# Optimization experiments

Hardware: AMD Instinct MI355X
Metric: run time of the kernel (lower is better)

The kernel has to match this reference:

```python
import jax, jax.numpy as jnp
import numpy as np

IM_H, IM_W = 128, 128
HT_H, HT_W = 184, 180
N_VOTES = 1_500_000
B, C = 4, 32


def setup_inputs() -> dict:
    key = jax.random.key(0)
    k1, k2, k3, k4 = jax.random.split(key, 4)
    input_im = jax.random.normal(k1, (B, C, IM_H, IM_W), dtype=jnp.float32)
    im_idx = jax.random.randint(k2, (N_VOTES,), 0, IM_H * IM_W, dtype=jnp.int32)
    ht_idx = jax.random.randint(k3, (N_VOTES,), 0, HT_H * HT_W, dtype=jnp.int32)
    weight = jax.random.uniform(k4, (N_VOTES,), dtype=jnp.float32)
    return {"input_im": input_im, "im_idx": im_idx, "ht_idx": ht_idx, "weight": weight}


def reference(input_im, im_idx, ht_idx, weight):
    # input_im: [B, C, H, W] -> flatten pixels
    b, c, h, w = input_im.shape
    x = input_im.reshape(b, c, h * w)
    # gather voting pixel values and apply vote weights: [B, C, N]
    votes = x[:, :, im_idx] * weight  # broadcast weight over B, C
    # scatter-add into Hough bins (segment over leading axis)
    data = votes.transpose(2, 0, 1).reshape(votes.shape[2], b * c)  # [N, B*C]
    ht = jax.ops.segment_sum(data, ht_idx, num_segments=HT_H * HT_W)  # [HT, B*C]
    out = ht.T.reshape(b, c, HT_H, HT_W)
    return out
```

## Files before the change

### kernel.cpp

```cpp
#include <hip/hip_runtime.h>


#define HW   16384
#define BC   128
#define NHT  33120
#define RB   60
#define NB   552
#define CAPB 3712
#define CAPR 3528
#define VPB  4096
#define OFL_CAP 8192

typedef int iv4 __attribute__((ext_vector_type(4)));

__device__ __forceinline__ unsigned short f2bf(float f) {
  unsigned int u = __float_as_uint(f);
  u = (u + 0x7fff + ((u >> 16) & 1)) >> 16;
  return (unsigned short)u;
}

__global__ void k_zero(int* __restrict__ gcur, int* __restrict__ ofl_cnt) {
  int i = blockIdx.x * blockDim.x + threadIdx.x;
  if (i < NB) gcur[i] = 0;
  if (i == NB) *ofl_cnt = 0;
}

__global__ void k_transpose_in(const float* __restrict__ in,
                               unsigned short* __restrict__ xTh) {
  __shared__ float tile[32][33];
  int hw0 = blockIdx.x * 32, bc0 = blockIdx.y * 32;
  int tx = threadIdx.x, ty = threadIdx.y;
#pragma unroll
  for (int k = 0; k < 32; k += 8)
    tile[ty + k][tx] = in[(size_t)(bc0 + ty + k) * HW + hw0 + tx];
  __syncthreads();
#pragma unroll
  for (int k = 0; k < 32; k += 8)
    xTh[(size_t)(hw0 + ty + k) * BC + bc0 + tx] = f2bf(tile[tx][ty + k]);
}

__global__ __launch_bounds__(1024) void k_bucket(
    const int* __restrict__ im, const int* __restrict__ ht,
    const float* __restrict__ wt, int n,
    int* __restrict__ gcur, int2* __restrict__ bkt,
    int* __restrict__ ofl_cnt, int2* __restrict__ ofl) {
  __shared__ int cnt[NB];
  __shared__ int base[NB];
  int tid = threadIdx.x;
  int i0 = blockIdx.x * VPB;
  for (int b = tid; b < NB; b += 1024) cnt[b] = 0;
  __syncthreads();
  int hv[4];
#pragma unroll
  for (int k = 0; k < 4; ++k) {
    int i = i0 + k * 1024 + tid;
    hv[k] = (i < n) ? ht[i] : -1;
    if (i < n) atomicAdd(&cnt[hv[k] / RB], 1);
  }
  __syncthreads();
  for (int b = tid; b < NB; b += 1024) {
    int c = cnt[b];
    base[b] = c ? atomicAdd(&gcur[b], c) : 0;
    cnt[b] = 0;
  }
  __syncthreads();
#pragma unroll
  for (int k = 0; k < 4; ++k) {
    int i = i0 + k * 1024 + tid;
    if (i < n) {
      int h = hv[k];
      int b = h / RB;
      int hl = h - b * RB;
      int pos = base[b] + atomicAdd(&cnt[b], 1);
      if (pos < CAPR) {
        bkt[(size_t)b * CAPB + pos] =
            make_int2((im[i] & 0x3FFF) | (hl << 14), __float_as_int(wt[i]));
      } else {
        int o = atomicAdd(ofl_cnt, 1);
        if (o < OFL_CAP)
          ofl[o] = make_int2((im[i] & 0x3FFF) | (h << 14), __float_as_int(wt[i]));
      }
    }
  }
}

__global__ __launch_bounds__(512) void k_resort(
    const int2* __restrict__ bkt, const int* __restrict__ gcur,
    int2* __restrict__ fsorted, int* __restrict__ foffs, int* __restrict__ fcnt) {
  __shared__ int2 buf[CAPB];
  __shared__ int hist[RB];
  __shared__ int off[RB];
  int r = blockIdx.x, tid = threadIdx.x;
  int n = gcur[r];
  if (n > CAPR) n = CAPR;
  const int2* s = bkt + (size_t)r * CAPB;
  for (int i = tid; i < n; i += 512) buf[i] = s[i];
  if (tid < RB) hist[tid] = 0;
  __syncthreads();
  for (int i = tid; i < n; i += 512)
    atomicAdd(&hist[buf[i].x >> 14], 1);
  __syncthreads();
  if (tid == 0) {
    int run = 0;
    for (int b = 0; b < RB; ++b) { off[b] = run; run += (hist[b] + 3) & ~3; }
  }
  __syncthreads();
  if (tid < RB) {
    int padded = (hist[tid] + 3) & ~3;
    foffs[r * RB + tid] = r * CAPB + off[tid];
    fcnt[r * RB + tid] = padded;
    for (int d = hist[tid]; d < padded; ++d)
      fsorted[(size_t)r * CAPB + off[tid] + d] = make_int2(0, 0);
    hist[tid] = 0;
  }
  __syncthreads();
  for (int i = tid; i < n; i += 512) {
    int2 v = buf[i];
    int hl = v.x >> 14;
    int pos = off[hl] + atomicAdd(&hist[hl], 1);
    fsorted[(size_t)r * CAPB + pos] = make_int2(v.x & 0x3FFF, v.y);
  }
}

__device__ __forceinline__ void pick4(iv4 a, iv4 b, int q, int& im, float& w) {
  int imx = (q & 2) ? b.x : a.x;
  int imz = (q & 2) ? b.z : a.z;
  im = (q & 1) ? imz : imx;
  int wx = (q & 2) ? b.y : a.y;
  int wz = (q & 2) ? b.w : a.w;
  w = __int_as_float((q & 1) ? wz : wx);
}

__global__ __launch_bounds__(256) void k_accum5(
    const int2* __restrict__ fsorted, const int* __restrict__ foffs,
    const int* __restrict__ fcnt, const unsigned short* __restrict__ xTh,
    float* __restrict__ outT) {
  int gid = blockIdx.x * blockDim.x + threadIdx.x;
  int bin = __builtin_amdgcn_readfirstlane(gid >> 6);
  if (bin >= NHT) return;
  int lane = threadIdx.x & 63;
  int q = lane >> 4;
  int cg = lane & 15;
  int start = foffs[bin], n = fcnt[bin];
  const int* s = (const int*)(fsorted + start);
  const unsigned short* xb = xTh + (cg << 3);
  float acc[8] = {0, 0, 0, 0, 0, 0, 0, 0};

#define GATHER_FMA(IM, W)                                                     \
  {                                                                           \
    iv4 xd = *(const iv4*)(xb + ((size_t)(IM) << 7));                         \
    _Pragma("unroll") for (int c = 0; c < 4; ++c) {                           \
      float lo = __uint_as_float(((unsigned int)xd[c]) << 16);                \
      float hi = __uint_as_float(((unsigned int)xd[c]) & 0xffff0000u);        \
      acc[2 * c]     = fmaf((W), lo, acc[2 * c]);                             \
      acc[2 * c + 1] = fmaf((W), hi, acc[2 * c + 1]);                         \
    }                                                                         \
  }

  int i = 0;
  for (; i + 8 <= n; i += 8) {
    iv4 r0 = __builtin_nontemporal_load((const iv4*)(s + 2 * i));
    iv4 r1 = __builtin_nontemporal_load((const iv4*)(s + 2 * i + 4));
    iv4 r2 = __builtin_nontemporal_load((const iv4*)(s + 2 * i + 8));
    iv4 r3 = __builtin_nontemporal_load((const iv4*)(s + 2 * i + 12));
    int im0; float w0; pick4(r0, r1, q, im0, w0);
    int im1; float w1; pick4(r2, r3, q, im1, w1);
    GATHER_FMA(im0, w0);
    GATHER_FMA(im1, w1);
  }
  for (; i < n; i += 4) {
    iv4 r0 = __builtin_nontemporal_load((const iv4*)(s + 2 * i));
    iv4 r1 = __builtin_nontemporal_load((const iv4*)(s + 2 * i + 4));
    int im0; float w0; pick4(r0, r1, q, im0, w0);
    GATHER_FMA(im0, w0);
  }
#undef GATHER_FMA

  float r[8];
#pragma unroll
  for (int k = 0; k < 8; ++k) {
    float t = acc[k] + __shfl_xor(acc[k], 16);
    r[k] = t + __shfl_xor(t, 32);
  }
  if (lane < 16) {
    float4 lo = {r[0], r[1], r[2], r[3]};
    float4 hi = {r[4], r[5], r[6], r[7]};
    float4* dst = (float4*)(outT + ((size_t)bin << 7) + (cg << 3));
    __builtin_nontemporal_store(lo.x, &((float*)dst)[0]);
    __builtin_nontemporal_store(lo.y, &((float*)dst)[1]);
    __builtin_nontemporal_store(lo.z, &((float*)dst)[2]);
    __builtin_nontemporal_store(lo.w, &((float*)dst)[3]);
    __builtin_nontemporal_store(hi.x, &((float*)dst)[4]);
    __builtin_nontemporal_store(hi.y, &((float*)dst)[5]);
    __builtin_nontemporal_store(hi.z, &((float*)dst)[6]);
    __builtin_nontemporal_store(hi.w, &((float*)dst)[7]);
  }
}

__global__ void k_transpose_out(const float* __restrict__ outT, float* __restrict__ out) {
  __shared__ float tile[32][33];
  int ht0 = blockIdx.x * 32, bc0 = blockIdx.y * 32;
  int tx = threadIdx.x, ty = threadIdx.y;
#pragma unroll
  for (int k = 0; k < 32; k += 8)
    tile[ty + k][tx] = outT[(size_t)(ht0 + ty + k) * BC + bc0 + tx];
  __syncthreads();
#pragma unroll
  for (int k = 0; k < 32; k += 8)
    out[(size_t)(bc0 + ty + k) * NHT + ht0 + tx] = tile[tx][ty + k];
}

__global__ void k_overflow(const int* __restrict__ ofl_cnt, const int2* __restrict__ ofl,
                           const unsigned short* __restrict__ xTh,
                           float* __restrict__ out) {
  int cnt = *ofl_cnt;
  if (cnt > OFL_CAP) cnt = OFL_CAP;
  int c = threadIdx.x;
  for (int v = blockIdx.x; v < cnt; v += gridDim.x) {
    int2 rec = ofl[v];
    int imv = rec.x & 0x3FFF, h = rec.x >> 14;
    float wv = __int_as_float(rec.y);
    float xv = __uint_as_float(((unsigned int)xTh[((size_t)imv << 7) + c]) << 16);
    atomicAdd(&out[(size_t)c * NHT + h], wv * xv);
  }
}

extern "C" void kernel_launch(void* const* d_in, const int* in_sizes, int n_in,
                              void* d_out, int out_size, void* d_ws, size_t ws_size,
                              hipStream_t stream) {
  const float* input_im = (const float*)d_in[0];
  const int*   im_idx   = (const int*)d_in[1];
  const int*   ht_idx   = (const int*)d_in[2];
  const float* weight   = (const float*)d_in[3];
  float*       out      = (float*)d_out;
  const int N = in_sizes[1];

  char* w = (char*)d_ws;
  unsigned short* xTh = (unsigned short*)(w + 0);
  int2*  bkt     = (int2*) (w + 4194304);
  int2*  fsorted = (int2*) (w + 20586496);
  float* outT    = (float*)(w + 36978688);
  int*   foffs   = (int*)  (w + 53936128);
  int*   fcnt    = (int*)  (w + 54068608);
  int*   gcur    = (int*)  (w + 54201088);
  int*   ofl_cnt = (int*)  (w + 54203392);
  int2*  ofl     = (int2*) (w + 54203520);

  k_zero<<<(NB + 256) / 256, 256, 0, stream>>>(gcur, ofl_cnt);
  k_transpose_in<<<dim3(HW / 32, BC / 32), dim3(32, 8), 0, stream>>>(input_im, xTh);
  k_bucket<<<(N + VPB - 1) / VPB, 1024, 0, stream>>>(im_idx, ht_idx, weight, N,
                                                     gcur, bkt, ofl_cnt, ofl);
  k_resort<<<NB, 512, 0, stream>>>(bkt, gcur, fsorted, foffs, fcnt);
  k_accum5<<<NHT * 64 / 256, 256, 0, stream>>>(fsorted, foffs, fcnt, xTh, outT);
  k_transpose_out<<<dim3(NHT / 32, BC / 32), dim3(32, 8), 0, stream>>>(outT, out);
  k_overflow<<<16, BC, 0, stream>>>(ofl_cnt, ofl, xTh, out);
}
```

Measured before the change: 152.9 us.

## Fuse accumulation with output transpose and overflow handling; merge zero and transpose-in

Merges the zeroing kernel into the input transpose kernel as an extra block. The accumulation kernel now handles 32 bins per block, collects the results in shared memory and writes the final [BC, NHT] layout directly. This removes the outT intermediate, the transpose-out kernel and the overflow kernel, cutting two launches and a round trip of roughly 17MB through memory. In exchange, every block scans the whole overflow list serially whenever it is non-empty, and there are fewer and larger blocks, each running 4 bins per wave in sequence, which reduces load balance.

After: 161.7 us. 1.06x slower.

```diff
diff --git a/kernel.cpp b/kernel.cpp
--- a/kernel.cpp
+++ b/kernel.cpp
@@ -19,16 +19,16 @@
   return (unsigned short)u;
 }
 
-__global__ void k_zero(int* __restrict__ gcur, int* __restrict__ ofl_cnt) {
-  int i = blockIdx.x * blockDim.x + threadIdx.x;
-  if (i < NB) gcur[i] = 0;
-  if (i == NB) *ofl_cnt = 0;
-}
-
-__global__ void k_transpose_in(const float* __restrict__ in,
-                               unsigned short* __restrict__ xTh) {
+__global__ void k_init(const float* __restrict__ in, unsigned short* __restrict__ xTh,
+                       int* __restrict__ gcur, int* __restrict__ ofl_cnt) {
+  if (blockIdx.x == 2048) {
+    int tid = threadIdx.y * 32 + threadIdx.x;
+    for (int i = tid; i < NB; i += 256) gcur[i] = 0;
+    if (tid == 0) *ofl_cnt = 0;
+    return;
+  }
   __shared__ float tile[32][33];
-  int hw0 = blockIdx.x * 32, bc0 = blockIdx.y * 32;
+  int hw0 = (blockIdx.x & 511) * 32, bc0 = (blockIdx.x >> 9) * 32;
   int tx = threadIdx.x, ty = threadIdx.y;
 #pragma unroll
   for (int k = 0; k < 32; k += 8)
@@ -131,20 +131,26 @@
   w = __int_as_float((q & 1) ? wz : wx);
 }
 
-__global__ __launch_bounds__(256) void k_accum5(
+__global__ __launch_bounds__(512) void k_accum6(
     const int2* __restrict__ fsorted, const int* __restrict__ foffs,
     const int* __restrict__ fcnt, const unsigned short* __restrict__ xTh,
-    float* __restrict__ outT) {
-  int gid = blockIdx.x * blockDim.x + threadIdx.x;
-  int bin = __builtin_amdgcn_readfirstlane(gid >> 6);
-  if (bin >= NHT) return;
-  int lane = threadIdx.x & 63;
+    float* __restrict__ out, const int* __restrict__ ofl_cnt,
+    const int2* __restrict__ ofl) {
+  __shared__ float lacc[32 * 129];
+  int tid = threadIdx.x;
+  int ht0 = blockIdx.x * 32;
+  int w = __builtin_amdgcn_readfirstlane(tid >> 6);
+  int lane = tid & 63;
   int q = lane >> 4;
   int cg = lane & 15;
-  int start = foffs[bin], n = fcnt[bin];
-  const int* s = (const int*)(fsorted + start);
   const unsigned short* xb = xTh + (cg << 3);
-  float acc[8] = {0, 0, 0, 0, 0, 0, 0, 0};
+
+#pragma unroll
+  for (int bi = 0; bi < 4; ++bi) {
+    int bin = ht0 + w * 4 + bi;
+    int start = foffs[bin], n = fcnt[bin];
+    const int* s = (const int*)(fsorted + start);
+    float acc[8] = {0, 0, 0, 0, 0, 0, 0, 0};
 
 #define GATHER_FMA(IM, W)                                                     \
   {                                                                           \
@@ -157,71 +163,61 @@
     }                                                                         \
   }
 
-  int i = 0;
-  for (; i + 8 <= n; i += 8) {
-    iv4 r0 = __builtin_nontemporal_load((const iv4*)(s + 2 * i));
-    iv4 r1 = __builtin_nontemporal_load((const iv4*)(s + 2 * i + 4));
-    iv4 r2 = __builtin_nontemporal_load((const iv4*)(s + 2 * i + 8));
-    iv4 r3 = __builtin_nontemporal_load((const iv4*)(s + 2 * i + 12));
-    int im0; float w0; pick4(r0, r1, q, im0, w0);
-    int im1; float w1; pick4(r2, r3, q, im1, w1);
-    GATHER_FMA(im0, w0);
-    GATHER_FMA(im1, w1);
-  }
-  for (; i < n; i += 4) {
-    iv4 r0 = __builtin_nontemporal_load((const iv4*)(s + 2 * i));
-    iv4 r1 = __builtin_nontemporal_load((const iv4*)(s + 2 * i + 4));
-    int im0; float w0; pick4(r0, r1, q, im0, w0);
-    GATHER_FMA(im0, w0);
-  }
+    int i = 0;
+    for (; i + 8 <= n; i += 8) {
+      iv4 r0 = __builtin_nontemporal_load((const iv4*)(s + 2 * i));
+      iv4 r1 = __builtin_nontemporal_load((const iv4*)(s + 2 * i + 4));
+      iv4 r2 = __builtin_nontemporal_load((const iv4*)(s + 2 * i + 8));
+      iv4 r3 = __builtin_nontemporal_load((const iv4*)(s + 2 * i + 12));
+      int im0; float w0; pick4(r0, r1, q, im0, w0);
+      int im1; float w1; pick4(r2, r3, q, im1, w1);
+      GATHER_FMA(im0, w0);
+      GATHER_FMA(im1, w1);
+    }
+    for (; i < n; i += 4) {
+      iv4 r0 = __builtin_nontemporal_load((const iv4*)(s + 2 * i));
+      iv4 r1 = __builtin_nontemporal_load((const iv4*)(s + 2 * i + 4));
+      int im0; float w0; pick4(r0, r1, q, im0, w0);
+      GATHER_FMA(im0, w0);
+    }
 #undef GATHER_FMA
 
-  float r[8];
+#pragma unroll
+    for (int k = 0; k < 8; ++k) {
+      float t = acc[k] + __shfl_xor(acc[k], 16);
+      acc[k] = t + __shfl_xor(t, 32);
+    }
+    if (lane < 16) {
+      int row = (w * 4 + bi) * 129 + (cg << 3);
+#pragma unroll
+      for (int k = 0; k < 8; ++k) lacc[row + k] = acc[k];
+    }
+  }
+  __syncthreads();
+
+  int cnt = *ofl_cnt;
+  if (cnt > 0) {
+    if (cnt > OFL_CAP) cnt = OFL_CAP;
+    if (tid < 128) {
+      for (int v = 0; v < cnt; ++v) {
+        int2 rec = ofl[v];
+        int h = rec.x >> 14;
+        if (h >= ht0 && h < ht0 + 32) {
+          int imv = rec.x & 0x3FFF;
+          float wv = __int_as_float(rec.y);
+          float xv = __uint_as_float(((unsigned int)xTh[((size_t)imv << 7) + tid]) << 16);
+          lacc[(h - ht0) * 129 + tid] += wv * xv;
+        }
+      }
+    }
+  }
+  __syncthreads();
+
 #pragma unroll
   for (int k = 0; k < 8; ++k) {
-    float t = acc[k] + __shfl_xor(acc[k], 16);
-    r[k] = t + __shfl_xor(t, 32);
-  }
-  if (lane < 16) {
-    float4 lo = {r[0], r[1], r[2], r[3]};
-    float4 hi = {r[4], r[5], r[6], r[7]};
-    float4* dst = (float4*)(outT + ((size_t)bin << 7) + (cg << 3));
-    __builtin_nontemporal_store(lo.x, &((float*)dst)[0]);
-    __builtin_nontemporal_store(lo.y, &((float*)dst)[1]);
-    __builtin_nontemporal_store(lo.z, &((float*)dst)[2]);
-    __builtin_nontemporal_store(lo.w, &((float*)dst)[3]);
-    __builtin_nontemporal_store(hi.x, &((float*)dst)[4]);
-    __builtin_nontemporal_store(hi.y, &((float*)dst)[5]);
-    __builtin_nontemporal_store(hi.z, &((float*)dst)[6]);
-    __builtin_nontemporal_store(hi.w, &((float*)dst)[7]);
-  }
-}
-
-__global__ void k_transpose_out(const float* __restrict__ outT, float* __restrict__ out) {
-  __shared__ float tile[32][33];
-  int ht0 = blockIdx.x * 32, bc0 = blockIdx.y * 32;
-  int tx = threadIdx.x, ty = threadIdx.y;
-#pragma unroll
-  for (int k = 0; k < 32; k += 8)
-    tile[ty + k][tx] = outT[(size_t)(ht0 + ty + k) * BC + bc0 + tx];
-  __syncthreads();
-#pragma unroll
-  for (int k = 0; k < 32; k += 8)
-    out[(size_t)(bc0 + ty + k) * NHT + ht0 + tx] = tile[tx][ty + k];
-}
-
-__global__ void k_overflow(const int* __restrict__ ofl_cnt, const int2* __restrict__ ofl,
-                           const unsigned short* __restrict__ xTh,
-                           float* __restrict__ out) {
-  int cnt = *ofl_cnt;
-  if (cnt > OFL_CAP) cnt = OFL_CAP;
-  int c = threadIdx.x;
-  for (int v = blockIdx.x; v < cnt; v += gridDim.x) {
-    int2 rec = ofl[v];
-    int imv = rec.x & 0x3FFF, h = rec.x >> 14;
-    float wv = __int_as_float(rec.y);
-    float xv = __uint_as_float(((unsigned int)xTh[((size_t)imv << 7) + c]) << 16);
-    atomicAdd(&out[(size_t)c * NHT + h], wv * xv);
+    int ch = k * 16 + (tid >> 5);
+    int j = tid & 31;
+    out[(size_t)ch * NHT + ht0 + j] = lacc[j * 129 + ch];
   }
 }
 
@@ -239,19 +235,16 @@
   unsigned short* xTh = (unsigned short*)(w + 0);
   int2*  bkt     = (int2*) (w + 4194304);
   int2*  fsorted = (int2*) (w + 20586496);
-  float* outT    = (float*)(w + 36978688);
-  int*   foffs   = (int*)  (w + 53936128);
-  int*   fcnt    = (int*)  (w + 54068608);
-  int*   gcur    = (int*)  (w + 54201088);
-  int*   ofl_cnt = (int*)  (w + 54203392);
-  int2*  ofl     = (int2*) (w + 54203520);
-
-  k_zero<<<(NB + 256) / 256, 256, 0, stream>>>(gcur, ofl_cnt);
-  k_transpose_in<<<dim3(HW / 32, BC / 32), dim3(32, 8), 0, stream>>>(input_im, xTh);
+  int*   foffs   = (int*)  (w + 36978688);
+  int*   fcnt    = (int*)  (w + 37111168);
+  int*   gcur    = (int*)  (w + 37243648);
+  int*   ofl_cnt = (int*)  (w + 37245952);
+  int2*  ofl     = (int2*) (w + 37246080);
+
+  k_init<<<2049, dim3(32, 8), 0, stream>>>(input_im, xTh, gcur, ofl_cnt);
   k_bucket<<<(N + VPB - 1) / VPB, 1024, 0, stream>>>(im_idx, ht_idx, weight, N,
                                                      gcur, bkt, ofl_cnt, ofl);
   k_resort<<<NB, 512, 0, stream>>>(bkt, gcur, fsorted, foffs, fcnt);
-  k_accum5<<<NHT * 64 / 256, 256, 0, stream>>>(fsorted, foffs, fcnt, xTh, outT);
-  k_transpose_out<<<dim3(NHT / 32, BC / 32), dim3(32, 8), 0, stream>>>(outT, out);
-  k_overflow<<<16, BC, 0, stream>>>(ofl_cnt, ofl, xTh, out);
-}
+  k_accum6<<<NHT / 32, 512, 0, stream>>>(fsorted, foffs, fcnt, xTh, out,
+                                         ofl_cnt, ofl);
+}
```
